# Optimization experiments

Measured on AMD Instinct MI355X. Metric: run time of the kernel, lower is better.

## Reference

```python
import jax, jax.numpy as jnp
import numpy as np

DIM = 1024
HEAD_DIM = 64
N_HEADS = DIM // HEAD_DIM  # 16
COND_DIM = 256
LENGTHS = (1, 4, 16, 64, 256, 1024)
SEQ = sum(LENGTHS)  # 1365
LN_EPS = 1e-5
ROT_D = 3 * (HEAD_DIM // 8)  # 24; 2*ROT_D = 48 <= HEAD_DIM


def _axial_pos(h, w):
    hp = np.linspace(-1.0, 1.0, h + 1); hp = (hp[:-1] + hp[1:]) / 2
    wp = np.linspace(-1.0, 1.0, w + 1); wp = (wp[:-1] + wp[1:]) / 2
    return np.stack(np.meshgrid(hp, wp, indexing='ij'), -1).reshape(h * w, 2)


def _make_theta():
    d = 5
    poses = []
    for i in range(d):
        pa = _axial_pos(32 >> i, 32 >> i)
        pr = np.full((pa.shape[0], 1), (d - i) / d)
        poses.insert(0, np.concatenate([pa, pr], -1))
    poses.insert(0, np.zeros((1, 3)))
    pos = np.concatenate(poses, 0)  # [1365, 3]
    log_min, log_max = np.log(np.pi), np.log(10 * np.pi)
    freqs = np.exp(np.linspace(log_min, log_max, HEAD_DIM // 8 * N_HEADS + 1)[:-1])
    freqs = freqs.reshape(HEAD_DIM // 8, N_HEADS).T  # [H, head_dim//8]
    th = pos[:, None, 0:1] * freqs  # [S, H, head_dim//8]
    tw = pos[:, None, 1:2] * freqs
    td = pos[:, None, 2:3] * freqs
    theta = np.concatenate([th, tw, td], -1)  # [S, H, ROT_D]
    return jnp.asarray(theta.transpose(1, 0, 2), dtype=jnp.float32)  # [H, S, ROT_D]


def _make_mask():
    m = np.zeros((SEQ, SEQ), dtype=bool)
    i = 0
    for L in LENGTHS:
        m[i:, i:i + L] = True
        i += L
    return jnp.asarray(m)


THETA = _make_theta()  # [H, S, ROT_D], constant buffer
MASK = _make_mask()    # [S, S] bool, constant buffer


def _rope(x, theta):
    # x: [B, H, S, head_dim]; theta: [H, S, ROT_D]
    d = theta.shape[-1]
    x1, x2, rest = x[..., :d], x[..., d:2 * d], x[..., 2 * d:]
    cos, sin = jnp.cos(theta), jnp.sin(theta)
    return jnp.concatenate([x1 * cos - x2 * sin, x2 * cos + x1 * sin, rest], -1)


def setup_inputs() -> dict:
    key = jax.random.key(0)
    ks = jax.random.split(key, 6)
    s = 0.02
    x = jax.random.normal(ks[0], (8, SEQ, DIM), jnp.float32)
    cond = jax.random.normal(ks[1], (8, 1, COND_DIM), jnp.float32)
    adaln_w = jax.random.normal(ks[2], (COND_DIM, 2 * DIM), jnp.float32) * s
    adaln_b = jnp.zeros((2 * DIM,), jnp.float32)
    qkv_w = jax.random.normal(ks[3], (DIM, 3 * DIM), jnp.float32) * s
    qkv_b = jnp.zeros((3 * DIM,), jnp.float32)
    out_w = jax.random.normal(ks[4], (DIM, DIM), jnp.float32) * s
    out_b = jnp.zeros((DIM,), jnp.float32)
    return {"x": x, "cond": cond, "adaln_w": adaln_w, "adaln_b": adaln_b,
            "qkv_w": qkv_w, "qkv_b": qkv_b, "out_w": out_w, "out_b": out_b}


def reference(x, cond, adaln_w, adaln_b, qkv_w, qkv_b, out_w, out_b):
    B, S, _ = x.shape
    skip = x
    # AdaLN: zero-init proj in the original; math is LN(x)*(w+1)+b
    wb = cond @ adaln_w + adaln_b  # [B, 1, 2*DIM]
    w, b = jnp.split(wb, 2, axis=-1)
    mu = x.mean(-1, keepdims=True)
    var = ((x - mu) ** 2).mean(-1, keepdims=True)
    xn = (x - mu) * jax.lax.rsqrt(var + LN_EPS)
    xn = xn * (w + 1.0) + b
    # QKV
    qkv = xn @ qkv_w + qkv_b  # [B, S, 3*DIM]
    qkv = qkv.reshape(B, S, 3, N_HEADS, HEAD_DIM).transpose(0, 3, 2, 1, 4)  # [B,H,3,S,hd]
    q, k, v = qkv[:, :, 0], qkv[:, :, 1], qkv[:, :, 2]
    theta = THETA[:, :S]  # [H, S, ROT_D]
    q = _rope(q, theta)
    k = _rope(k, theta)
    # block-causal masked SDPA
    scores = jnp.einsum('bhqd,bhkd->bhqk', q, k) / np.sqrt(HEAD_DIM).astype(np.float32)
    scores = jnp.where(MASK[:S, :S], scores, -1e30)
    attn = jax.nn.softmax(scores, axis=-1)
    o = jnp.einsum('bhqk,bhkd->bhqd', attn, v)
    o = o.transpose(0, 2, 1, 3).reshape(B, S, DIM)
    return o @ out_w + out_b + skip
```

## Files before the change

### kernel.cpp

```cpp
#include <hip/hip_runtime.h>
#include <math.h>


typedef unsigned short u16;
typedef unsigned short u16x8 __attribute__((ext_vector_type(8)));
typedef unsigned short u16x4 __attribute__((ext_vector_type(4)));
typedef __bf16        bf16x8 __attribute__((ext_vector_type(8)));
typedef float         f32x4  __attribute__((ext_vector_type(4)));

#define SEQ  1365
#define SP   1408
#define BHN  128
#define MTOT 10920
#define DIMN 1024
#define QSCALE 0.1803368801111204f

__device__ __forceinline__ u16 f2bf(float x){
  unsigned r; asm("v_cvt_pk_bf16_f32 %0, %1, %1" : "=v"(r) : "v"(x));
  return (u16)r;
}
__device__ __forceinline__ unsigned cvtpk(float a, float b){
  unsigned r; asm("v_cvt_pk_bf16_f32 %0, %1, %2" : "=v"(r) : "v"(a), "v"(b));
  return r;
}
__device__ __forceinline__ float bf2f(u16 b){
  return __builtin_bit_cast(float, ((unsigned)b) << 16);
}
__device__ __forceinline__ bf16x8 ldbf8(const u16* p){
  return __builtin_bit_cast(bf16x8, *(const u16x8*)p);
}
__device__ __forceinline__ f32x4 mfma16(bf16x8 a, bf16x8 b, f32x4 c){
  return __builtin_amdgcn_mfma_f32_16x16x32_bf16(a, b, c, 0, 0, 0);
}
__device__ __forceinline__ void gload16(const u16* g, u16* l){
  __builtin_amdgcn_global_load_lds(
      (const __attribute__((address_space(1))) void*)(g),
      (__attribute__((address_space(3))) void*)(l), 16, 0, 0);
}

__global__ __launch_bounds__(256) void transpose_bf16(const float* __restrict__ in,
                                                      u16* __restrict__ outT,
                                                      int K, int N){
  __shared__ float tile[32][33];
  const int tx = threadIdx.x & 31, ty = threadIdx.x >> 5;
  const int n0 = blockIdx.x*32, k0 = blockIdx.y*32;
#pragma unroll
  for (int i=0;i<32;i+=8) tile[ty+i][tx] = in[(size_t)(k0+ty+i)*N + n0+tx];
  __syncthreads();
#pragma unroll
  for (int i=0;i<32;i+=8) outT[(size_t)(n0+ty+i)*K + k0+tx] = f2bf(tile[tx][ty+i]);
}

__global__ __launch_bounds__(256) void adaln_kernel(const float* __restrict__ cond,
                                                    const float* __restrict__ w,
                                                    const float* __restrict__ bsrc,
                                                    float* __restrict__ wb){
  __shared__ float cs[256];
  const int bt = blockIdx.x >> 3, ch = blockIdx.x & 7;
  const int t = threadIdx.x;
  cs[t] = cond[bt*256 + t];
  __syncthreads();
  const int n = ch*256 + t;
  float acc = bsrc[n];
  for (int j=0;j<256;j++) acc += cs[j] * w[(size_t)j*2048 + n];
  wb[bt*2048 + n] = acc;
}

__global__ __launch_bounds__(256) void theta_kernel(float* __restrict__ ctab,
                                                    float* __restrict__ stab){
  int idx = blockIdx.x*256 + threadIdx.x;
  if (idx >= 16*SEQ*24) return;
  int c = idx % 24;
  int rest = idx / 24;
  int s = rest % SEQ;
  int h = rest / SEQ;
  float p0 = 0.f, p1 = 0.f, p2 = 0.f;
  if (s >= 1){
    int start, sh; float pr;
    if      (s <   5){start=1;   sh=1; pr=0.2f;}
    else if (s <  21){start=5;   sh=2; pr=0.4f;}
    else if (s <  85){start=21;  sh=3; pr=0.6f;}
    else if (s < 341){start=85;  sh=4; pr=0.8f;}
    else             {start=341; sh=5; pr=1.0f;}
    int n = s - start;
    int row = n >> sh, colp = n & ((1<<sh)-1);
    float g = (float)(1 << sh);
    p0 = -1.f + (2*row+1)/g;
    p1 = -1.f + (2*colp+1)/g;
    p2 = pr;
  }
  int j = c & 7, comp = c >> 3;
  float kf = (float)(j*16 + h);
  float freq = 3.14159265358979323846f * exp2f(kf * (3.3219280948873623f/128.f));
  float pos = (comp==0) ? p0 : ((comp==1) ? p1 : p2);
  float th = pos * freq;
  ctab[idx] = cosf(th);
  stab[idx] = sinf(th);
}

__global__ __launch_bounds__(256) void ln_kernel(const float* __restrict__ x,
                                                 const float* __restrict__ wb,
                                                 u16* __restrict__ xn){
  const int row = blockIdx.x;
  const int b = row / SEQ;
  const int t = threadIdx.x, w = t>>6, l = t&63;
  const float4 v = ((const float4*)(x + (size_t)row*DIMN))[t];
  float s = v.x + v.y + v.z + v.w;
#pragma unroll
  for (int m=1; m<64; m<<=1) s += __shfl_xor(s, m);
  __shared__ float red1[4], red2[4];
  if (l == 0) red1[w] = s;
  __syncthreads();
  float mean = (red1[0]+red1[1]+red1[2]+red1[3]) * (1.f/1024.f);
  float dx = v.x-mean, dy = v.y-mean, dz = v.z-mean, dw = v.w-mean;
  float q = dx*dx + dy*dy + dz*dz + dw*dw;
#pragma unroll
  for (int m=1; m<64; m<<=1) q += __shfl_xor(q, m);
  if (l == 0) red2[w] = q;
  __syncthreads();
  float var = (red2[0]+red2[1]+red2[2]+red2[3]) * (1.f/1024.f);
  float rs = rsqrtf(var + 1e-5f);
  const float* wrow = wb + b*2048;
  int n0 = t*4;
  u16x4 o;
  o[0] = f2bf(dx*rs*(wrow[n0+0]+1.f) + wrow[1024+n0+0]);
  o[1] = f2bf(dy*rs*(wrow[n0+1]+1.f) + wrow[1024+n0+1]);
  o[2] = f2bf(dz*rs*(wrow[n0+2]+1.f) + wrow[1024+n0+2]);
  o[3] = f2bf(dw*rs*(wrow[n0+3]+1.f) + wrow[1024+n0+3]);
  *(u16x4*)&xn[(size_t)row*DIMN + n0] = o;
}

__global__ __launch_bounds__(256) void gemm_qkv(const u16* __restrict__ A,
                                                const u16* __restrict__ BT,
                                                const float* __restrict__ bias,
                                                u16* __restrict__ qb, u16* __restrict__ kb,
                                                u16* __restrict__ vb){
  __shared__ u16 As[128*32];
  __shared__ u16 Bs[128*32];
  const int K = 1024;
  const int t = threadIdx.x, l = t & 63, w = t >> 6, lr = l & 15, lg = l >> 4;
  const int wr = (w>>1)*64, wc = (w&1)*64;
  const int bm = blockIdx.y*128, bn = blockIdx.x*128;

  f32x4 acc[4][4];
#pragma unroll
  for (int mi=0;mi<4;mi++)
#pragma unroll
    for (int ni=0;ni<4;ni++) acc[mi][ni] = (f32x4){0.f,0.f,0.f,0.f};

  const int srow = l >> 2;
  const int scol = (l & 3) << 3;

  for (int k0=0; k0<K; k0+=32){
    __syncthreads();
#pragma unroll
    for (int j=0;j<2;j++){
      int rb = (w*2+j)*16;
      int gr = bm + rb + srow; if (gr >= MTOT) gr = MTOT-1;
      gload16(&A[(size_t)gr*K + k0 + scol], &As[rb*32]);
      gload16(&BT[(size_t)(bn + rb + srow)*K + k0 + scol], &Bs[rb*32]);
    }
    __syncthreads();
    bf16x8 af[4], bfr[4];
#pragma unroll
    for (int mi=0;mi<4;mi++) af[mi] = ldbf8(&As[(wr+mi*16+lr)*32 + lg*8]);
#pragma unroll
    for (int ni=0;ni<4;ni++) bfr[ni] = ldbf8(&Bs[(wc+ni*16+lr)*32 + lg*8]);
#pragma unroll
    for (int mi=0;mi<4;mi++)
#pragma unroll
      for (int ni=0;ni<4;ni++)
        acc[mi][ni] = mfma16(af[mi], bfr[ni], acc[mi][ni]);
  }

#pragma unroll
  for (int mi=0;mi<4;mi++)
#pragma unroll
    for (int ni=0;ni<4;ni++){
      int col = bn + wc + ni*16 + lr;
      float bia = bias[col];
      int three = col >> 10, rem = col & 1023;
      int h = rem >> 6, d = rem & 63;
      float scl = (three == 0) ? QSCALE : 1.0f;
#pragma unroll
      for (int r=0;r<4;r++){
        int m = bm + wr + mi*16 + lg*4 + r;
        if (m < MTOT){
          int b = m / SEQ; int s = m - b*SEQ;
          u16 val = f2bf((acc[mi][ni][r] + bia) * scl);
          int bh = b*16 + h;
          if (three == 0)      qb[((size_t)bh*SP + s)*64 + d] = val;
          else if (three == 1) kb[((size_t)bh*SP + s)*64 + d] = val;
          else                 vb[((size_t)bh*64 + d)*SP + s] = val;
        }
      }
    }
}

__global__ __launch_bounds__(256) void rope2_kernel(u16* __restrict__ qb,
                                                    u16* __restrict__ kb,
                                                    const float* __restrict__ ctab,
                                                    const float* __restrict__ stab){
  int rid = blockIdx.x*256 + threadIdx.x;
  if (rid >= BHN*SEQ) return;
  int bh = rid / SEQ, s = rid - bh*SEQ, h = bh & 15;
  const float* cp = ctab + (size_t)(h*SEQ + s)*24;
  const float* sp = stab + (size_t)(h*SEQ + s)*24;
  float cs[24], sn[24];
#pragma unroll
  for (int i=0;i<6;i++){
    ((float4*)cs)[i] = ((const float4*)cp)[i];
    ((float4*)sn)[i] = ((const float4*)sp)[i];
  }
  size_t base = ((size_t)bh*SP + s)*64;
  u16 buf[48];
#pragma unroll
  for (int i=0;i<6;i++) ((u16x8*)buf)[i] = *(const u16x8*)&qb[base + i*8];
#pragma unroll
  for (int j=0;j<24;j++){
    float x1 = bf2f(buf[j]), x2 = bf2f(buf[24+j]);
    buf[j]    = f2bf(x1*cs[j] - x2*sn[j]);
    buf[24+j] = f2bf(x2*cs[j] + x1*sn[j]);
  }
#pragma unroll
  for (int i=0;i<6;i++) *(u16x8*)&qb[base + i*8] = ((u16x8*)buf)[i];
#pragma unroll
  for (int i=0;i<6;i++) ((u16x8*)buf)[i] = *(const u16x8*)&kb[base + i*8];
#pragma unroll
  for (int j=0;j<24;j++){
    float x1 = bf2f(buf[j]), x2 = bf2f(buf[24+j]);
    buf[j]    = f2bf(x1*cs[j] - x2*sn[j]);
    buf[24+j] = f2bf(x2*cs[j] + x1*sn[j]);
  }
#pragma unroll
  for (int i=0;i<6;i++) *(u16x8*)&kb[base + i*8] = ((u16x8*)buf)[i];
}

__global__ __launch_bounds__(256) void attn_kernel(const u16* __restrict__ qb,
                                                   const u16* __restrict__ kb,
                                                   const u16* __restrict__ vb,
                                                   u16* __restrict__ ob){
  __shared__ u16 Ks[64*72];
  __shared__ u16 Vs[64*72];
  __shared__ u16 Ps[128*72];
  const int bx = blockIdx.x;
  const int qt = (bx < 9) ? (bx + 2) : (bx - 9);
  const int bh = blockIdx.y;
  const int t = threadIdx.x, w = t>>6, l = t&63, lr = l&15, lg = l>>4, lg4 = lg<<2;
  const u16* qB = qb + (size_t)bh*SP*64;
  const u16* kB = kb + (size_t)bh*SP*64;
  const u16* vB = vb + (size_t)bh*64*SP;
  const int q0 = qt*128 + w*32;

  bf16x8 qf[2][2];
#pragma unroll
  for (int ni=0; ni<2; ni++)
#pragma unroll
    for (int kk=0; kk<2; kk++)
      qf[ni][kk] = ldbf8(&qB[(size_t)(q0+ni*16+lr)*64 + kk*32 + lg*8]);
  const int qg0 = q0 + lr, qg1 = q0 + 16 + lr;

  f32x4 oacc[2][4];
#pragma unroll
  for (int mo=0;mo<2;mo++)
#pragma unroll
    for (int nd=0;nd<4;nd++) oacc[mo][nd] = (f32x4){0.f,0.f,0.f,0.f};
  float lst[2] = {0.f, 0.f};

  int qmax = min(qt*128+127, SEQ-1);
  int kend = (qmax<1)?1:(qmax<5)?5:(qmax<21)?21:(qmax<85)?85:(qmax<341)?341:SEQ;
  int nkt = (kend + 63) >> 6;

  for (int kt=0; kt<nkt; kt++){
    const int kbase = kt*64;
    __syncthreads();
#pragma unroll
    for (int j=0;j<2;j++){
      int flat = t + j*256;
      int row = flat >> 3, kc = (flat & 7) << 3;
      *(u16x8*)&Ks[row*72+kc] = *(const u16x8*)&kB[(size_t)(kbase+row)*64 + kc];
      *(u16x8*)&Vs[row*72+kc] = *(const u16x8*)&vB[(size_t)row*SP + kbase + kc];
    }
    __syncthreads();

    f32x4 sacc[4][2];
#pragma unroll
    for (int mi=0;mi<4;mi++){
      sacc[mi][0] = (f32x4){0.f,0.f,0.f,0.f};
      sacc[mi][1] = (f32x4){0.f,0.f,0.f,0.f};
    }
#pragma unroll
    for (int mi=0;mi<4;mi++){
      bf16x8 k0f = ldbf8(&Ks[(mi*16+lr)*72 + lg*8]);
      bf16x8 k1f = ldbf8(&Ks[(mi*16+lr)*72 + 32 + lg*8]);
      sacc[mi][0] = mfma16(k0f, qf[0][0], sacc[mi][0]);
      sacc[mi][0] = mfma16(k1f, qf[0][1], sacc[mi][0]);
      sacc[mi][1] = mfma16(k0f, qf[1][0], sacc[mi][1]);
      sacc[mi][1] = mfma16(k1f, qf[1][1], sacc[mi][1]);
    }

    int lastk = kbase + 63;
    int visLast = (lastk>=SEQ)?(1<<30):(lastk>=341)?341:(lastk>=85)?85:
                  (lastk>=21)?21:(lastk>=5)?5:(lastk>=1)?1:0;
    if (visLast > q0){
#pragma unroll
      for (int mi=0;mi<4;mi++){
        int kv = kbase + mi*16 + lg4;
#pragma unroll
        for (int r=0;r<4;r++){
          int key = kv + r;
          int visv = (key>=SEQ)?(1<<30):(key>=341)?341:(key>=85)?85:
                     (key>=21)?21:(key>=5)?5:(key>=1)?1:0;
          if (qg0 < visv) sacc[mi][0][r] = -1e30f;
          if (qg1 < visv) sacc[mi][1][r] = -1e30f;
        }
      }
    }

    float pa[2] = {0.f, 0.f}, pb[2] = {0.f, 0.f};
#pragma unroll
    for (int mi=0;mi<4;mi++)
#pragma unroll
      for (int ni=0;ni<2;ni++){
        float p0 = __builtin_amdgcn_exp2f(sacc[mi][ni][0]);
        float p1 = __builtin_amdgcn_exp2f(sacc[mi][ni][1]);
        float p2 = __builtin_amdgcn_exp2f(sacc[mi][ni][2]);
        float p3 = __builtin_amdgcn_exp2f(sacc[mi][ni][3]);
        pa[ni] += p0 + p1;
        pb[ni] += p2 + p3;
        uint2 pk = { cvtpk(p0, p1), cvtpk(p2, p3) };
        *(uint2*)&Ps[(w*32+ni*16+lr)*72 + mi*16 + lg4] = pk;
      }
#pragma unroll
    for (int ni=0;ni<2;ni++){
      float s = pa[ni] + pb[ni];
      s += __shfl_xor(s, 16);
      s += __shfl_xor(s, 32);
      lst[ni] += s;
    }

    bf16x8 pf[2][2];
#pragma unroll
    for (int mo=0;mo<2;mo++)
#pragma unroll
      for (int kk=0;kk<2;kk++)
        pf[mo][kk] = ldbf8(&Ps[(w*32+mo*16+lr)*72 + kk*32 + lg*8]);
#pragma unroll
    for (int nd=0;nd<4;nd++){
      bf16x8 v0 = ldbf8(&Vs[(nd*16+lr)*72 + lg*8]);
      bf16x8 v1 = ldbf8(&Vs[(nd*16+lr)*72 + 32 + lg*8]);
#pragma unroll
      for (int mo=0;mo<2;mo++){
        oacc[mo][nd] = mfma16(pf[mo][0], v0, oacc[mo][nd]);
        oacc[mo][nd] = mfma16(pf[mo][1], v1, oacc[mo][nd]);
      }
    }
  }

  const int b = bh >> 4, h = bh & 15;
  float linv[2][4];
#pragma unroll
  for (int mo=0;mo<2;mo++)
#pragma unroll
    for (int r=0;r<4;r++)
      linv[mo][r] = 1.f / __shfl(lst[mo], lg4 + r);
#pragma unroll
  for (int mo=0;mo<2;mo++)
#pragma unroll
    for (int r=0;r<4;r++){
      int p = q0 + mo*16 + lg4 + r;
      if (p < SEQ){
#pragma unroll
        for (int nd=0;nd<4;nd++)
          ob[((size_t)(b*SEQ + p))*DIMN + h*64 + nd*16 + lr] = f2bf(oacc[mo][nd][r] * linv[mo][r]);
      }
    }
}

__global__ __launch_bounds__(256) void gemm_out(const u16* __restrict__ A,
                                                const u16* __restrict__ BT,
                                                const float* __restrict__ bias,
                                                const float* __restrict__ skip,
                                                float* __restrict__ out){
  __shared__ u16 As[128*32];
  __shared__ u16 Bs[128*32];
  const int K = 1024;
  const int t = threadIdx.x, l = t & 63, w = t >> 6, lr = l & 15, lg = l >> 4;
  const int wr = (w>>1)*64, wc = (w&1)*64;
  const int bm = blockIdx.y*128, bn = blockIdx.x*128;

  f32x4 acc[4][4];
#pragma unroll
  for (int mi=0;mi<4;mi++)
#pragma unroll
    for (int ni=0;ni<4;ni++) acc[mi][ni] = (f32x4){0.f,0.f,0.f,0.f};

  const int srow = l >> 2;
  const int scol = (l & 3) << 3;

  for (int k0=0; k0<K; k0+=32){
    __syncthreads();
#pragma unroll
    for (int j=0;j<2;j++){
      int rb = (w*2+j)*16;
      int gr = bm + rb + srow; if (gr >= MTOT) gr = MTOT-1;
      gload16(&A[(size_t)gr*K + k0 + scol], &As[rb*32]);
      gload16(&BT[(size_t)(bn + rb + srow)*K + k0 + scol], &Bs[rb*32]);
    }
    __syncthreads();
    bf16x8 af[4], bfr[4];
#pragma unroll
    for (int mi=0;mi<4;mi++) af[mi] = ldbf8(&As[(wr+mi*16+lr)*32 + lg*8]);
#pragma unroll
    for (int ni=0;ni<4;ni++) bfr[ni] = ldbf8(&Bs[(wc+ni*16+lr)*32 + lg*8]);
#pragma unroll
    for (int mi=0;mi<4;mi++)
#pragma unroll
      for (int ni=0;ni<4;ni++)
        acc[mi][ni] = mfma16(af[mi], bfr[ni], acc[mi][ni]);
  }

#pragma unroll
  for (int mi=0;mi<4;mi++)
#pragma unroll
    for (int ni=0;ni<4;ni++){
      int col = bn + wc + ni*16 + lr;
      float bia = bias[col];
#pragma unroll
      for (int r=0;r<4;r++){
        int m = bm + wr + mi*16 + lg*4 + r;
        if (m < MTOT){
          size_t idx = (size_t)m*DIMN + col;
          out[idx] = acc[mi][ni][r] + bia + skip[idx];
        }
      }
    }
}

extern "C" void kernel_launch(void* const* d_in, const int* in_sizes, int n_in,
                              void* d_out, int out_size, void* d_ws, size_t ws_size,
                              hipStream_t stream) {
  (void)in_sizes; (void)n_in; (void)out_size; (void)ws_size;
  const float* x        = (const float*)d_in[0];
  const float* cond     = (const float*)d_in[1];
  const float* adaln_w  = (const float*)d_in[2];
  const float* adaln_b  = (const float*)d_in[3];
  const float* qkv_w    = (const float*)d_in[4];
  const float* qkv_b    = (const float*)d_in[5];
  const float* out_w    = (const float*)d_in[6];
  const float* out_b    = (const float*)d_in[7];
  float* out = (float*)d_out;

  char* ws = (char*)d_ws;
  size_t off = 0;
  auto alloc = [&](size_t bytes)->void*{
    void* p = ws + off;
    off += (bytes + 255) & ~(size_t)255;
    return p;
  };
  float* wb     = (float*)alloc((size_t)8*2048*4);
  u16*   xn     = (u16*)  alloc((size_t)MTOT*DIMN*2);
  u16*   qkv_wT = (u16*)  alloc((size_t)3072*1024*2);
  u16*   out_wT = (u16*)  alloc((size_t)1024*1024*2);
  u16*   qbuf   = (u16*)  alloc((size_t)BHN*SP*64*2);
  u16*   kbuf   = (u16*)  alloc((size_t)BHN*SP*64*2);
  u16*   vbuf   = (u16*)  alloc((size_t)BHN*SP*64*2);
  float* ctab   = (float*)alloc((size_t)16*SEQ*24*4);
  float* stab   = (float*)alloc((size_t)16*SEQ*24*4);
  u16*   obuf   = xn;

  transpose_bf16<<<dim3(3072/32, 1024/32), 256, 0, stream>>>(qkv_w, qkv_wT, 1024, 3072);
  transpose_bf16<<<dim3(1024/32, 1024/32), 256, 0, stream>>>(out_w, out_wT, 1024, 1024);
  theta_kernel<<<(16*SEQ*24 + 255)/256, 256, 0, stream>>>(ctab, stab);
  adaln_kernel<<<64, 256, 0, stream>>>(cond, adaln_w, adaln_b, wb);
  ln_kernel<<<MTOT, 256, 0, stream>>>(x, wb, xn);
  gemm_qkv<<<dim3(3072/128, (MTOT+127)/128), 256, 0, stream>>>(xn, qkv_wT, qkv_b, qbuf, kbuf, vbuf);
  rope2_kernel<<<(BHN*SEQ + 255)/256, 256, 0, stream>>>(qbuf, kbuf, ctab, stab);
  attn_kernel<<<dim3((SEQ+127)/128, BHN), 256, 0, stream>>>(qbuf, kbuf, vbuf, obuf);
  gemm_out<<<dim3(1024/128, (MTOT+127)/128), 256, 0, stream>>>(obuf, out_wT, out_b, x, out);
}
```

Baseline: 432.0 us.

## Double GEMM K-tile with XOR-swizzled LDS and write V row-major then transpose

Both GEMMs now stage 64-wide K tiles instead of 32, which halves the number of barrier pairs per tile. An XOR swizzle on the LDS chunk index is meant to avoid bank conflicts on fragment reads. The QKV epilogue now writes V row-major like Q and K, replacing the strided transposed scatter. A new vtrans kernel then builds the transposed V layout the attention kernel expects, at the cost of an extra launch and a full V read/write pass. LDS use per block doubles, which may lower occupancy.

```diff
diff --git a/kernel.cpp b/kernel.cpp
--- a/kernel.cpp
+++ b/kernel.cpp
@@ -135,8 +135,8 @@
                                                 const float* __restrict__ bias,
                                                 u16* __restrict__ qb, u16* __restrict__ kb,
                                                 u16* __restrict__ vb){
-  __shared__ u16 As[128*32];
-  __shared__ u16 Bs[128*32];
+  __shared__ u16 As[128*64];
+  __shared__ u16 Bs[128*64];
   const int K = 1024;
   const int t = threadIdx.x, l = t & 63, w = t >> 6, lr = l & 15, lg = l >> 4;
   const int wr = (w>>1)*64, wc = (w&1)*64;
@@ -148,51 +148,54 @@
 #pragma unroll
     for (int ni=0;ni<4;ni++) acc[mi][ni] = (f32x4){0.f,0.f,0.f,0.f};
 
-  const int srow = l >> 2;
-  const int scol = (l & 3) << 3;
-
-  for (int k0=0; k0<K; k0+=32){
+  const int srow8 = l >> 3;
+  const int scol  = ((l & 7) ^ srow8) << 3;
+  const int sw0   = (lr & 7);
+
+  for (int k0=0; k0<K; k0+=64){
     __syncthreads();
 #pragma unroll
-    for (int j=0;j<2;j++){
-      int rb = (w*2+j)*16;
-      int gr = bm + rb + srow; if (gr >= MTOT) gr = MTOT-1;
-      gload16(&A[(size_t)gr*K + k0 + scol], &As[rb*32]);
-      gload16(&BT[(size_t)(bn + rb + srow)*K + k0 + scol], &Bs[rb*32]);
+    for (int j=0;j<4;j++){
+      int rb = (w*4 + j)*8;
+      int gr = bm + rb + srow8; if (gr >= MTOT) gr = MTOT-1;
+      gload16(&A[(size_t)gr*K + k0 + scol], &As[rb*64]);
+      gload16(&BT[(size_t)(bn + rb + srow8)*K + k0 + scol], &Bs[rb*64]);
     }
     __syncthreads();
-    bf16x8 af[4], bfr[4];
-#pragma unroll
-    for (int mi=0;mi<4;mi++) af[mi] = ldbf8(&As[(wr+mi*16+lr)*32 + lg*8]);
-#pragma unroll
-    for (int ni=0;ni<4;ni++) bfr[ni] = ldbf8(&Bs[(wc+ni*16+lr)*32 + lg*8]);
-#pragma unroll
-    for (int mi=0;mi<4;mi++)
-#pragma unroll
-      for (int ni=0;ni<4;ni++)
-        acc[mi][ni] = mfma16(af[mi], bfr[ni], acc[mi][ni]);
+#pragma unroll
+    for (int kk=0;kk<2;kk++){
+      const int ch = ((kk*4 + lg) ^ sw0) << 3;
+      bf16x8 af[4], bfr[4];
+#pragma unroll
+      for (int mi=0;mi<4;mi++) af[mi] = ldbf8(&As[(wr+mi*16+lr)*64 + ch]);
+#pragma unroll
+      for (int ni=0;ni<4;ni++) bfr[ni] = ldbf8(&Bs[(wc+ni*16+lr)*64 + ch]);
+#pragma unroll
+      for (int mi=0;mi<4;mi++)
+#pragma unroll
+        for (int ni=0;ni<4;ni++)
+          acc[mi][ni] = mfma16(af[mi], bfr[ni], acc[mi][ni]);
+    }
   }
 
 #pragma unroll
   for (int mi=0;mi<4;mi++)
 #pragma unroll
-    for (int ni=0;ni<4;ni++){
-      int col = bn + wc + ni*16 + lr;
-      float bia = bias[col];
-      int three = col >> 10, rem = col & 1023;
-      int h = rem >> 6, d = rem & 63;
-      float scl = (three == 0) ? QSCALE : 1.0f;
-#pragma unroll
-      for (int r=0;r<4;r++){
-        int m = bm + wr + mi*16 + lg*4 + r;
-        if (m < MTOT){
-          int b = m / SEQ; int s = m - b*SEQ;
-          u16 val = f2bf((acc[mi][ni][r] + bia) * scl);
-          int bh = b*16 + h;
-          if (three == 0)      qb[((size_t)bh*SP + s)*64 + d] = val;
-          else if (three == 1) kb[((size_t)bh*SP + s)*64 + d] = val;
-          else                 vb[((size_t)bh*64 + d)*SP + s] = val;
-        }
+    for (int r=0;r<4;r++){
+      int m = bm + wr + mi*16 + lg*4 + r;
+      if (m >= MTOT) continue;
+      int b = m / SEQ; int s = m - b*SEQ;
+      size_t rowbase = ((size_t)(b*16)*SP + s)*64;
+#pragma unroll
+      for (int ni=0;ni<4;ni++){
+        int col = bn + wc + ni*16 + lr;
+        int three = col >> 10, rem = col & 1023;
+        int h = rem >> 6, d = rem & 63;
+        float v = acc[mi][ni][r] + bias[col];
+        size_t idx = rowbase + (size_t)h*SP*64 + d;
+        if (three == 0)      qb[idx] = f2bf(v * QSCALE);
+        else if (three == 1) kb[idx] = f2bf(v);
+        else                 vb[idx] = f2bf(v);
       }
     }
 }
@@ -234,6 +237,30 @@
   }
 #pragma unroll
   for (int i=0;i<6;i++) *(u16x8*)&kb[base + i*8] = ((u16x8*)buf)[i];
+}
+
+__global__ __launch_bounds__(256) void vtrans_kernel(const u16* __restrict__ vb,
+                                                     u16* __restrict__ vT){
+  __shared__ u16 tile[64][72];
+  const int st = blockIdx.x*64, bh = blockIdx.y;
+  const int r = threadIdx.x >> 3, c8 = (threadIdx.x & 7)*8;
+  const u16* src = vb + ((size_t)bh*SP + st)*64;
+#pragma unroll
+  for (int j=0;j<2;j++){
+    int row = r + j*32;
+    *(u16x8*)&tile[row][c8] = *(const u16x8*)&src[(size_t)row*64 + c8];
+  }
+  __syncthreads();
+  u16* dst = vT + (size_t)bh*64*SP + st;
+#pragma unroll
+  for (int j=0;j<2;j++){
+    int d = r + j*32;
+    u16x8 tmp;
+#pragma unroll
+    for (int i=0;i<8;i++)
+      tmp[i] = (st + c8 + i < SEQ) ? tile[c8+i][d] : (u16)0;
+    *(u16x8*)&dst[(size_t)d*SP + c8] = tmp;
+  }
 }
 
 __global__ __launch_bounds__(256) void attn_kernel(const u16* __restrict__ qb,
@@ -382,8 +409,8 @@
                                                 const float* __restrict__ bias,
                                                 const float* __restrict__ skip,
                                                 float* __restrict__ out){
-  __shared__ u16 As[128*32];
-  __shared__ u16 Bs[128*32];
+  __shared__ u16 As[128*64];
+  __shared__ u16 Bs[128*64];
   const int K = 1024;
   const int t = threadIdx.x, l = t & 63, w = t >> 6, lr = l & 15, lg = l >> 4;
   const int wr = (w>>1)*64, wc = (w&1)*64;
@@ -395,29 +422,34 @@
 #pragma unroll
     for (int ni=0;ni<4;ni++) acc[mi][ni] = (f32x4){0.f,0.f,0.f,0.f};
 
-  const int srow = l >> 2;
-  const int scol = (l & 3) << 3;
-
-  for (int k0=0; k0<K; k0+=32){
+  const int srow8 = l >> 3;
+  const int scol  = ((l & 7) ^ srow8) << 3;
+  const int sw0   = (lr & 7);
+
+  for (int k0=0; k0<K; k0+=64){
     __syncthreads();
 #pragma unroll
-    for (int j=0;j<2;j++){
-      int rb = (w*2+j)*16;
-      int gr = bm + rb + srow; if (gr >= MTOT) gr = MTOT-1;
-      gload16(&A[(size_t)gr*K + k0 + scol], &As[rb*32]);
-      gload16(&BT[(size_t)(bn + rb + srow)*K + k0 + scol], &Bs[rb*32]);
+    for (int j=0;j<4;j++){
+      int rb = (w*4 + j)*8;
+      int gr = bm + rb + srow8; if (gr >= MTOT) gr = MTOT-1;
+      gload16(&A[(size_t)gr*K + k0 + scol], &As[rb*64]);
+      gload16(&BT[(size_t)(bn + rb + srow8)*K + k0 + scol], &Bs[rb*64]);
     }
     __syncthreads();
-    bf16x8 af[4], bfr[4];
-#pragma unroll
-    for (int mi=0;mi<4;mi++) af[mi] = ldbf8(&As[(wr+mi*16+lr)*32 + lg*8]);
-#pragma unroll
-    for (int ni=0;ni<4;ni++) bfr[ni] = ldbf8(&Bs[(wc+ni*16+lr)*32 + lg*8]);
-#pragma unroll
-    for (int mi=0;mi<4;mi++)
-#pragma unroll
-      for (int ni=0;ni<4;ni++)
-        acc[mi][ni] = mfma16(af[mi], bfr[ni], acc[mi][ni]);
+#pragma unroll
+    for (int kk=0;kk<2;kk++){
+      const int ch = ((kk*4 + lg) ^ sw0) << 3;
+      bf16x8 af[4], bfr[4];
+#pragma unroll
+      for (int mi=0;mi<4;mi++) af[mi] = ldbf8(&As[(wr+mi*16+lr)*64 + ch]);
+#pragma unroll
+      for (int ni=0;ni<4;ni++) bfr[ni] = ldbf8(&Bs[(wc+ni*16+lr)*64 + ch]);
+#pragma unroll
+      for (int mi=0;mi<4;mi++)
+#pragma unroll
+        for (int ni=0;ni<4;ni++)
+          acc[mi][ni] = mfma16(af[mi], bfr[ni], acc[mi][ni]);
+    }
   }
 
 #pragma unroll
@@ -465,6 +497,7 @@
   u16*   qbuf   = (u16*)  alloc((size_t)BHN*SP*64*2);
   u16*   kbuf   = (u16*)  alloc((size_t)BHN*SP*64*2);
   u16*   vbuf   = (u16*)  alloc((size_t)BHN*SP*64*2);
+  u16*   vTbuf  = (u16*)  alloc((size_t)BHN*SP*64*2);
   float* ctab   = (float*)alloc((size_t)16*SEQ*24*4);
   float* stab   = (float*)alloc((size_t)16*SEQ*24*4);
   u16*   obuf   = xn;
@@ -476,6 +509,7 @@
   ln_kernel<<<MTOT, 256, 0, stream>>>(x, wb, xn);
   gemm_qkv<<<dim3(3072/128, (MTOT+127)/128), 256, 0, stream>>>(xn, qkv_wT, qkv_b, qbuf, kbuf, vbuf);
   rope2_kernel<<<(BHN*SEQ + 255)/256, 256, 0, stream>>>(qbuf, kbuf, ctab, stab);
-  attn_kernel<<<dim3((SEQ+127)/128, BHN), 256, 0, stream>>>(qbuf, kbuf, vbuf, obuf);
+  vtrans_kernel<<<dim3(SP/64, BHN), 256, 0, stream>>>(vbuf, vTbuf);
+  attn_kernel<<<dim3((SEQ+127)/128, BHN), 256, 0, stream>>>(qbuf, kbuf, vTbuf, obuf);
   gemm_out<<<dim3(1024/128, (MTOT+127)/128), 256, 0, stream>>>(obuf, out_wT, out_b, x, out);
 }
```

Measured after the change: 482.0 us. 1.12x slower.
